# Kernel tuning notes

Hardware: AMD Instinct MI355X
Metric: run time of the kernel (lower is better)

Reference implementation:

```python
import jax, jax.numpy as jnp
import numpy as np

EMBED_DIM = 4096
NUM_HEADS = 64
RANK = 1
B, T = 64, 64  # T must equal NUM_HEADS for the mask broadcast (faithful to source)


def setup_inputs() -> dict:
    key = jax.random.key(0)
    k1, k2, k3, k4, k5 = jax.random.split(key, 5)
    C = EMBED_DIM
    s = 0.02
    return {
        "x": jax.random.normal(k1, (B, T, C), dtype=jnp.float32),
        "W_atten": jax.random.normal(k2, (3 * C, C), dtype=jnp.float32) * s,
        "b_atten": jax.random.normal(k3, (3 * C,), dtype=jnp.float32) * s,
        "W_proj": jax.random.normal(k4, (C, C), dtype=jnp.float32) * s,
        "b_proj": jax.random.normal(k5, (C,), dtype=jnp.float32) * s,
    }


def reference(x, W_atten, b_atten, W_proj, b_proj):
    Bx, Tx, C = x.shape
    H = NUM_HEADS
    hd = C // H
    r = RANK
    qkv = jnp.einsum("btc,oc->bto", x, W_atten) + b_atten  # (B,T,3C)
    q, k, v = jnp.split(qkv, 3, axis=2)
    # view (B,T,rank,H,hd) then transpose(1,2) -> (B,rank,T,H,hd)
    def reshp(t):
        return t.reshape(Bx, Tx, r, H, hd).transpose(0, 2, 1, 3, 4)
    q, k, v = reshp(q), reshp(k), reshp(v)
    scale = (1.0 / np.sqrt(hd)) * (r ** 0.5)
    # attention across heads at each timestep: (B,rank,T,H,H)
    att = jnp.einsum("brtqd,brtkd->brtqk", q, k) * scale
    # tril[:T,:T] broadcasts onto trailing (H,H) dims (requires T == H)
    tril = jnp.tril(jnp.ones((Tx, Tx), dtype=jnp.float32))
    att = jnp.where(tril == 0, -jnp.inf, att)
    att = jax.nn.softmax(att, axis=-1)
    y = jnp.einsum("brtqk,brtkd->brtqd", att, v)  # (B,rank,T,H,hd)
    y = y.transpose(0, 2, 1, 3, 4).reshape(Bx, Tx, C)
    return jnp.einsum("btc,oc->bto", y, W_proj) + b_proj
```

## Files before the change

kernel.cpp:

```cpp
#include <hip/hip_runtime.h>
#include <stdint.h>

#define M_TOK   4096
#define C_DIM   4096
#define N_QKV   12288
#define KD      4096
#define NT2     32

typedef __bf16 bf16x8 __attribute__((ext_vector_type(8)));
typedef float  f32x4  __attribute__((ext_vector_type(4)));
typedef unsigned short ushort8 __attribute__((ext_vector_type(8)));

__device__ __forceinline__ unsigned short f2bf(float f) {
  unsigned int u = __builtin_bit_cast(unsigned int, f);
  u = (u + 0x7FFFu + ((u >> 16) & 1u)) >> 16;
  return (unsigned short)u;
}

__global__ __launch_bounds__(256) void cvt_f32_bf16(const float* __restrict__ in,
                                                    unsigned short* __restrict__ out,
                                                    int n16) {
  int idx = blockIdx.x * 256 + threadIdx.x;
  if (idx >= n16) return;
  const float4* p = (const float4*)in;
  float4 a = p[idx * 2], b = p[idx * 2 + 1];
  uint4 r;
  r.x = (unsigned)f2bf(a.x) | ((unsigned)f2bf(a.y) << 16);
  r.y = (unsigned)f2bf(a.z) | ((unsigned)f2bf(a.w) << 16);
  r.z = (unsigned)f2bf(b.x) | ((unsigned)f2bf(b.y) << 16);
  r.w = (unsigned)f2bf(b.z) | ((unsigned)f2bf(b.w) << 16);
  ((uint4*)out)[idx] = r;
}

#define GLLDS(gp, lp) \
  __builtin_amdgcn_global_load_lds((const __attribute__((address_space(1))) unsigned int*)(gp), \
                                   (__attribute__((address_space(3))) unsigned int*)(lp), 16, 0, 0)


#define STAGE_A(buf, hf, tau) do {                                         \
    const unsigned short* g_ = Ag + (size_t)((hf) * 64) * KD + (tau) * 64; \
    unsigned short* d_ = As + (buf) * 16384 + (hf) * 8192 + t * 8;         \
    GLLDS(g_, d_);                                                         \
    GLLDS(g_ + (size_t)128 * KD, d_ + 4096);                               \
  } while (0)

#define STAGE_B(buf, nhf, tau) do {                                         \
    const unsigned short* g_ = Bg + (size_t)((nhf) * 32) * KD + (tau) * 64; \
    unsigned short* d_ = Bs + (buf) * 16384 + (nhf) * 8192 + t * 8;         \
    GLLDS(g_, d_);                                                          \
    GLLDS(g_ + (size_t)128 * KD, d_ + 4096);                                \
  } while (0)

#define LDA2_(buf, mh, bank) do {                                                 \
    const unsigned short* pa_ = As + (buf) * 16384 + (mh) * 8192 + wm * 4096 + lr * 64; \
    bank[0][0] = *(const bf16x8*)(pa_ + 0 * 1024 + ck0);                          \
    bank[0][1] = *(const bf16x8*)(pa_ + 1 * 1024 + ck0);                          \
    bank[0][2] = *(const bf16x8*)(pa_ + 2 * 1024 + ck0);                          \
    bank[0][3] = *(const bf16x8*)(pa_ + 3 * 1024 + ck0);                          \
    bank[1][0] = *(const bf16x8*)(pa_ + 0 * 1024 + ck1);                          \
    bank[1][1] = *(const bf16x8*)(pa_ + 1 * 1024 + ck1);                          \
    bank[1][2] = *(const bf16x8*)(pa_ + 2 * 1024 + ck1);                          \
    bank[1][3] = *(const bf16x8*)(pa_ + 3 * 1024 + ck1);                          \
  } while (0)

#define LDB_(buf, nhf, dst) do {                                                  \
    const unsigned short* pb_ = Bs + (buf) * 16384 + (nhf) * 8192 + wn * 2048 + lr * 64; \
    dst[0][0] = *(const bf16x8*)(pb_ + 0 * 1024 + ck0);                           \
    dst[0][1] = *(const bf16x8*)(pb_ + 1 * 1024 + ck0);                           \
    dst[1][0] = *(const bf16x8*)(pb_ + 0 * 1024 + ck1);                           \
    dst[1][1] = *(const bf16x8*)(pb_ + 1 * 1024 + ck1);                           \
  } while (0)

#define QUAD_(mh, nhf, abank, bsrc) do {                                          \
    __builtin_amdgcn_s_setprio(1);                                                \
    _Pragma("unroll") for (int kk_ = 0; kk_ < 2; ++kk_)                           \
    _Pragma("unroll") for (int mt_ = 0; mt_ < 4; ++mt_)                           \
    _Pragma("unroll") for (int nt_ = 0; nt_ < 2; ++nt_)                           \
      acc[mh][nhf][mt_][nt_] = __builtin_amdgcn_mfma_f32_16x16x32_bf16(           \
          abank[kk_][mt_], bsrc[kk_][nt_], acc[mh][nhf][mt_][nt_], 0, 0, 0);      \
    __builtin_amdgcn_s_setprio(0);                                                \
  } while (0)

#define SB_()  __builtin_amdgcn_sched_barrier(0)
#define BAR_() do { asm volatile("" ::: "memory");  __builtin_amdgcn_s_barrier(); \
                    asm volatile("" ::: "memory"); } while (0)
#define LGKM0_() do { asm volatile("s_waitcnt lgkmcnt(0)" ::: "memory"); SB_(); } while (0)
#define LGKM8_() do { asm volatile("s_waitcnt lgkmcnt(8)" ::: "memory"); SB_(); } while (0)
#define VM6_()   asm volatile("s_waitcnt vmcnt(6)" ::: "memory")

template <int OUT_BF16>
__global__ __launch_bounds__(512, 2) void gemm256(const unsigned short* __restrict__ A,
                                                  const unsigned short* __restrict__ B,
                                                  const float* __restrict__ bias,
                                                  void* __restrict__ Cptr,
                                                  int N) {
  __shared__ __align__(16) unsigned short As[32768];
  __shared__ __align__(16) unsigned short Bs[32768];

  const int t   = threadIdx.x;
  const int nwg = gridDim.x;
  const int bid = blockIdx.x;
  const int wg  = (bid & 7) * (nwg >> 3) + (bid >> 3);
  const int bm  = wg & 15;
  const int bn  = wg >> 4;

  const int w  = t >> 6, l = t & 63;
  const int wm = w >> 2, wn = w & 3;
  const int lr = l & 15, lq = l >> 4;
  const int ck0 = (lq ^ (lr & 7)) * 8;
  const int ck1 = ck0 ^ 32;

  const int r8  = t >> 3;
  const int kcs = ((t & 7) ^ (r8 & 7)) * 8;
  const unsigned short* Ag = A + (size_t)(bm * 256 + r8) * KD + kcs;
  const unsigned short* Bg = B + (size_t)(bn * 256 + ((t >> 8) << 6) + (r8 & 31)) * KD + kcs;

  f32x4 acc[2][2][4][2] = {};
  bf16x8 afk0[2][4], afk1[2][4], bA[2][2], bB[2][2];

  STAGE_A(0, 0, 0); STAGE_B(0, 0, 0); STAGE_B(0, 1, 0); STAGE_A(0, 1, 0);
  STAGE_A(1, 0, 1); STAGE_B(1, 0, 1); STAGE_B(1, 1, 1);
  VM6_();
  BAR_();

#pragma unroll 1
  for (int i = 0; i < NT2; ++i) {
    const int t1 = 2 * i + 1;
    const int t2 = (2 * i + 2 < 64) ? 2 * i + 2 : 63;
    const int t3 = (2 * i + 3 < 64) ? 2 * i + 3 : 63;

    SB_();
    LDA2_(0, 0, afk0);
    LDB_(0, 0, bA);
    SB_();
    STAGE_A(1, 1, t1);
    BAR_();
    LGKM0_();
    QUAD_(0, 0, afk0, bA);
    SB_();
    BAR_();
    SB_();
    LDB_(0, 1, bB);
    SB_();
    LDA2_(0, 1, afk1);
    SB_();
    STAGE_A(0, 0, t2);
    BAR_();
    LGKM8_();
    QUAD_(0, 1, afk0, bB);
    SB_();
    BAR_();
    STAGE_B(0, 0, t2);
    BAR_();
    LGKM0_();
    QUAD_(1, 1, afk1, bB);
    SB_();
    BAR_();
    STAGE_B(0, 1, t2);
    BAR_();
    SB_();
    QUAD_(1, 0, afk1, bA);
    SB_();
    VM6_();
    BAR_();

    SB_();
    LDA2_(1, 0, afk0);
    LDB_(1, 0, bA);
    SB_();
    STAGE_A(0, 1, t2);
    BAR_();
    LGKM0_();
    QUAD_(0, 0, afk0, bA);
    SB_();
    BAR_();
    SB_();
    LDB_(1, 1, bB);
    SB_();
    LDA2_(1, 1, afk1);
    SB_();
    STAGE_A(1, 0, t3);
    BAR_();
    LGKM8_();
    QUAD_(0, 1, afk0, bB);
    SB_();
    BAR_();
    STAGE_B(1, 0, t3);
    BAR_();
    LGKM0_();
    QUAD_(1, 1, afk1, bB);
    SB_();
    BAR_();
    STAGE_B(1, 1, t3);
    BAR_();
    SB_();
    QUAD_(1, 0, afk1, bA);
    SB_();
    VM6_();
    BAR_();
  }

  asm volatile("s_waitcnt vmcnt(0)" ::: "memory");

  const int row0 = bm * 256 + wm * 128 + lq * 4;
  const int col0 = bn * 256 + wn * 64 + lr;
#pragma unroll
  for (int nhf = 0; nhf < 2; ++nhf)
#pragma unroll
    for (int nt = 0; nt < 2; ++nt) {
      const int col = col0 + nhf * 32 + nt * 16;
      const float bv = bias[col];
#pragma unroll
      for (int mh = 0; mh < 2; ++mh)
#pragma unroll
        for (int mt = 0; mt < 4; ++mt) {
          const int row = row0 + mh * 64 + mt * 16;
#pragma unroll
          for (int rg = 0; rg < 4; ++rg) {
            float v = acc[mh][nhf][mt][nt][rg] + bv;
            if (OUT_BF16)
              ((unsigned short*)Cptr)[(size_t)(row + rg) * N + col] = f2bf(v);
            else
              ((float*)Cptr)[(size_t)(row + rg) * N + col] = v;
          }
        }
    }
}

#define AST 72

__global__ __launch_bounds__(64) void attn_mfma(const unsigned short* __restrict__ qkv,
                                                unsigned short* __restrict__ y) {
  __shared__ __align__(16) unsigned short Ks[64 * AST];
  __shared__ __align__(16) unsigned short Vs[64 * AST];
  const int l  = threadIdx.x;
  const int lr = l & 15;
  const int lq = l >> 4;
  const size_t base = (size_t)blockIdx.x * 12288;

  {
    const int jr = l >> 3;
    const int cc = (l & 7) * 8;
#pragma unroll
    for (int c = 0; c < 8; ++c) {
      const int j = c * 8 + jr;
      *(uint4*)(Ks + j * AST + cc) = *(const uint4*)(qkv + base + 4096 + (size_t)j * 64 + cc);
      *(uint4*)(Vs + j * AST + cc) = *(const uint4*)(qkv + base + 8192 + (size_t)j * 64 + cc);
    }
  }

  bf16x8 aq[4][2];
#pragma unroll
  for (int it = 0; it < 4; ++it)
#pragma unroll
    for (int kk = 0; kk < 2; ++kk)
      aq[it][kk] = *(const bf16x8*)(qkv + base + (size_t)(it * 16 + lr) * 64 + kk * 32 + lq * 8);

  __syncthreads();

  f32x4 acc[4][4] = {};
#pragma unroll
  for (int kk = 0; kk < 2; ++kk) {
    bf16x8 bk[4];
#pragma unroll
    for (int jt = 0; jt < 4; ++jt)
      bk[jt] = *(const bf16x8*)(Ks + (jt * 16 + lr) * AST + kk * 32 + lq * 8);
#pragma unroll
    for (int it = 0; it < 4; ++it)
#pragma unroll
      for (int jt = 0; jt < 4; ++jt)
        acc[it][jt] = __builtin_amdgcn_mfma_f32_16x16x32_bf16(aq[it][kk], bk[jt], acc[it][jt], 0, 0, 0);
  }

#pragma unroll
  for (int it = 0; it < 4; ++it) {
#pragma unroll
    for (int rg = 0; rg < 4; ++rg) {
      const int row = it * 16 + lq * 4 + rg;
      float mx = -1e30f;
#pragma unroll
      for (int jt = 0; jt < 4; ++jt) {
        const int col = jt * 16 + lr;
        float s = acc[it][jt][rg] * 0.125f;
        s = (col <= row) ? s : -1e30f;
        acc[it][jt][rg] = s;
        mx = fmaxf(mx, s);
      }
#pragma unroll
      for (int d = 1; d < 16; d <<= 1)
        mx = fmaxf(mx, __shfl_xor(mx, d));
      float sum = 0.f;
#pragma unroll
      for (int jt = 0; jt < 4; ++jt) {
        float e = __expf(acc[it][jt][rg] - mx);
        acc[it][jt][rg] = e;
        sum += e;
      }
#pragma unroll
      for (int d = 1; d < 16; d <<= 1)
        sum += __shfl_xor(sum, d);
      const float inv = 1.f / sum;
#pragma unroll
      for (int jt = 0; jt < 4; ++jt)
        acc[it][jt][rg] *= inv;
    }
  }

#pragma unroll
  for (int it = 0; it < 4; ++it)
#pragma unroll
    for (int rg = 0; rg < 4; ++rg) {
      const int row = it * 16 + lq * 4 + rg;
#pragma unroll
      for (int jt = 0; jt < 4; ++jt)
        Ks[row * AST + jt * 16 + lr] = f2bf(acc[it][jt][rg]);
    }
  __syncthreads();

  f32x4 out[4][4] = {};
#pragma unroll
  for (int kk = 0; kk < 2; ++kk) {
    bf16x8 ap[4];
#pragma unroll
    for (int it = 0; it < 4; ++it)
      ap[it] = *(const bf16x8*)(Ks + (it * 16 + lr) * AST + kk * 32 + lq * 8);
#pragma unroll
    for (int dt = 0; dt < 4; ++dt) {
      ushort8 vt;
#pragma unroll
      for (int jj = 0; jj < 8; ++jj)
        vt[jj] = Vs[(kk * 32 + lq * 8 + jj) * AST + dt * 16 + lr];
      const bf16x8 bv = __builtin_bit_cast(bf16x8, vt);
#pragma unroll
      for (int it = 0; it < 4; ++it)
        out[it][dt] = __builtin_amdgcn_mfma_f32_16x16x32_bf16(ap[it], bv, out[it][dt], 0, 0, 0);
    }
  }

  unsigned short* yrow = y + (size_t)blockIdx.x * 4096;
#pragma unroll
  for (int it = 0; it < 4; ++it)
#pragma unroll
    for (int rg = 0; rg < 4; ++rg) {
      const int i = it * 16 + lq * 4 + rg;
#pragma unroll
      for (int dt = 0; dt < 4; ++dt)
        yrow[i * 64 + dt * 16 + lr] = f2bf(out[it][dt][rg]);
    }
}

extern "C" void kernel_launch(void* const* d_in, const int* in_sizes, int n_in,
                              void* d_out, int out_size, void* d_ws, size_t ws_size,
                              hipStream_t stream) {
  const float* x  = (const float*)d_in[0];
  const float* Wa = (const float*)d_in[1];
  const float* ba = (const float*)d_in[2];
  const float* Wp = (const float*)d_in[3];
  const float* bp = (const float*)d_in[4];
  float* out = (float*)d_out;

  unsigned short* regA = (unsigned short*)d_ws;
  unsigned short* regB = regA + (size_t)16777216;
  unsigned short* regC = regB + (size_t)50331648;
  unsigned short* xb   = regA;
  unsigned short* Wab  = regB;
  unsigned short* qkvb = regC;
  unsigned short* Wpb  = regA;
  unsigned short* yb   = regB;

  cvt_f32_bf16<<<(16777216 / 8) / 256, 256, 0, stream>>>(x, xb, 16777216 / 8);
  cvt_f32_bf16<<<(50331648 / 8) / 256, 256, 0, stream>>>(Wa, Wab, 50331648 / 8);

  gemm256<1><<<dim3((M_TOK / 256) * (N_QKV / 256)), dim3(512), 0, stream>>>(
      xb, Wab, ba, (void*)qkvb, N_QKV);

  cvt_f32_bf16<<<(16777216 / 8) / 256, 256, 0, stream>>>(Wp, Wpb, 16777216 / 8);

  attn_mfma<<<M_TOK, 64, 0, stream>>>(qkvb, yb);

  gemm256<0><<<dim3((M_TOK / 256) * (C_DIM / 256)), dim3(512), 0, stream>>>(
      yb, Wpb, bp, (void*)out, C_DIM);
}
```

Measured before the change: 884.6 us.

## Software-pipeline LDS fragment reads one MFMA quadrant ahead in GEMM main loop

Restructures the GEMM main loop so the LDS-to-register reads for the next quadrant are issued before the current quadrant's MFMAs. Partial lgkmcnt waits (4 or 8) replace full drains, and the barriers per half-iteration drop from about eight to four. The goal is to hide LDS read latency behind matrix math and cut synchronisation stalls. In exchange it uses more register pressure and depends on fragile ordering of the waitcnt values against the buffer reuse.

Result: slower. 926.0 us (+4.7%).

```diff
diff --git a/kernel.cpp b/kernel.cpp
--- a/kernel.cpp
+++ b/kernel.cpp
@@ -51,7 +51,7 @@
     GLLDS(g_ + (size_t)128 * KD, d_ + 4096);                                \
   } while (0)
 
-#define LDA2_(buf, mh, bank) do {                                                 \
+#define RD_A(buf, mh, bank) do {                                                  \
     const unsigned short* pa_ = As + (buf) * 16384 + (mh) * 8192 + wm * 4096 + lr * 64; \
     bank[0][0] = *(const bf16x8*)(pa_ + 0 * 1024 + ck0);                          \
     bank[0][1] = *(const bf16x8*)(pa_ + 1 * 1024 + ck0);                          \
@@ -63,7 +63,7 @@
     bank[1][3] = *(const bf16x8*)(pa_ + 3 * 1024 + ck1);                          \
   } while (0)
 
-#define LDB_(buf, nhf, dst) do {                                                  \
+#define RD_B(buf, nhf, dst) do {                                                  \
     const unsigned short* pb_ = Bs + (buf) * 16384 + (nhf) * 8192 + wn * 2048 + lr * 64; \
     dst[0][0] = *(const bf16x8*)(pb_ + 0 * 1024 + ck0);                           \
     dst[0][1] = *(const bf16x8*)(pb_ + 1 * 1024 + ck0);                           \
@@ -81,11 +81,11 @@
     __builtin_amdgcn_s_setprio(0);                                                \
   } while (0)
 
-#define SB_()  __builtin_amdgcn_sched_barrier(0)
-#define BAR_() do { asm volatile("" ::: "memory");  __builtin_amdgcn_s_barrier(); \
-                    asm volatile("" ::: "memory"); } while (0)
-#define LGKM0_() do { asm volatile("s_waitcnt lgkmcnt(0)" ::: "memory"); SB_(); } while (0)
+#define SB_()   __builtin_amdgcn_sched_barrier(0)
+#define BAR_()  do { asm volatile("" ::: "memory"); __builtin_amdgcn_s_barrier(); \
+                     asm volatile("" ::: "memory"); } while (0)
 #define LGKM8_() do { asm volatile("s_waitcnt lgkmcnt(8)" ::: "memory"); SB_(); } while (0)
+#define LGKM4_() do { asm volatile("s_waitcnt lgkmcnt(4)" ::: "memory"); SB_(); } while (0)
 #define VM6_()   asm volatile("s_waitcnt vmcnt(6)" ::: "memory")
 
 template <int OUT_BF16>
@@ -116,91 +116,68 @@
   const unsigned short* Bg = B + (size_t)(bn * 256 + ((t >> 8) << 6) + (r8 & 31)) * KD + kcs;
 
   f32x4 acc[2][2][4][2] = {};
-  bf16x8 afk0[2][4], afk1[2][4], bA[2][2], bB[2][2];
+  bf16x8 A0[2][4], A1[2][4], Bl[2][2], Bh[2][2];
 
   STAGE_A(0, 0, 0); STAGE_B(0, 0, 0); STAGE_B(0, 1, 0); STAGE_A(0, 1, 0);
   STAGE_A(1, 0, 1); STAGE_B(1, 0, 1); STAGE_B(1, 1, 1);
   VM6_();
   BAR_();
+  RD_A(0, 0, A0); RD_B(0, 0, Bl);
 
 #pragma unroll 1
   for (int i = 0; i < NT2; ++i) {
-    const int t1 = 2 * i + 1;
-    const int t2 = (2 * i + 2 < 64) ? 2 * i + 2 : 63;
-    const int t3 = (2 * i + 3 < 64) ? 2 * i + 3 : 63;
-
-    SB_();
-    LDA2_(0, 0, afk0);
-    LDB_(0, 0, bA);
-    SB_();
-    STAGE_A(1, 1, t1);
-    BAR_();
-    LGKM0_();
-    QUAD_(0, 0, afk0, bA);
-    SB_();
-    BAR_();
-    SB_();
-    LDB_(0, 1, bB);
-    SB_();
-    LDA2_(0, 1, afk1);
-    SB_();
-    STAGE_A(0, 0, t2);
-    BAR_();
+    const int tS1e = 2 * i + 1;
+    const int te2  = (2 * i + 2 < 64) ? 2 * i + 2 : 63;
+    const int to2  = (2 * i + 3 < 64) ? 2 * i + 3 : 63;
+
+    STAGE_A(1, 1, tS1e);
+    RD_A(0, 1, A1);
     LGKM8_();
-    QUAD_(0, 1, afk0, bB);
-    SB_();
-    BAR_();
-    STAGE_B(0, 0, t2);
-    BAR_();
-    LGKM0_();
-    QUAD_(1, 1, afk1, bB);
-    SB_();
-    BAR_();
-    STAGE_B(0, 1, t2);
-    BAR_();
-    SB_();
-    QUAD_(1, 0, afk1, bA);
-    SB_();
+    QUAD_(0, 0, A0, Bl);
+    BAR_();
+    STAGE_A(0, 0, te2);
+    RD_B(0, 1, Bh);
+    LGKM4_();
+    QUAD_(1, 0, A1, Bl);
     VM6_();
     BAR_();
-
-    SB_();
-    LDA2_(1, 0, afk0);
-    LDB_(1, 0, bA);
-    SB_();
-    STAGE_A(0, 1, t2);
-    BAR_();
-    LGKM0_();
-    QUAD_(0, 0, afk0, bA);
-    SB_();
-    BAR_();
-    SB_();
-    LDB_(1, 1, bB);
-    SB_();
-    LDA2_(1, 1, afk1);
-    SB_();
-    STAGE_A(1, 0, t3);
-    BAR_();
+    STAGE_B(0, 0, te2);
+    RD_B(1, 0, Bl);
+    LGKM4_();
+    QUAD_(1, 1, A1, Bh);
+    BAR_();
+    STAGE_B(0, 1, te2);
+    RD_A(1, 0, A1);
     LGKM8_();
-    QUAD_(0, 1, afk0, bB);
-    SB_();
-    BAR_();
-    STAGE_B(1, 0, t3);
-    BAR_();
-    LGKM0_();
-    QUAD_(1, 1, afk1, bB);
-    SB_();
-    BAR_();
-    STAGE_B(1, 1, t3);
-    BAR_();
-    SB_();
-    QUAD_(1, 0, afk1, bA);
-    SB_();
+    QUAD_(0, 1, A0, Bh);
     VM6_();
     BAR_();
-  }
-
-  asm volatile("s_waitcnt vmcnt(0)" ::: "memory");
+
+    STAGE_A(0, 1, te2);
+    RD_A(1, 1, A0);
+    LGKM8_();
+    QUAD_(0, 0, A1, Bl);
+    BAR_();
+    STAGE_A(1, 0, to2);
+    RD_B(1, 1, Bh);
+    LGKM4_();
+    QUAD_(1, 0, A0, Bl);
+    VM6_();
+    BAR_();
+    STAGE_B(1, 0, to2);
+    RD_B(0, 0, Bl);
+    LGKM4_();
+    QUAD_(1, 1, A0, Bh);
+    BAR_();
+    STAGE_B(1, 1, to2);
+    RD_A(0, 0, A0);
+    LGKM8_();
+    QUAD_(0, 1, A1, Bh);
+    VM6_();
+    BAR_();
+  }
+
+  asm volatile("s_waitcnt vmcnt(0) lgkmcnt(0)" ::: "memory");
 
   const int row0 = bm * 256 + wm * 128 + lq * 4;
   const int col0 = bn * 256 + wn * 64 + lr;
```
